# Kernel tuning notes

Hardware: AMD Instinct MI355X
Metric: run time of the kernel (lower is better)

## Reference

```python
import math
import jax, jax.numpy as jnp
import numpy as np

TOP_K, NC, ALPHA, BETA, EPS = 10, 80, 0.5, 6.0, 1e-9
IMG, STRIDES = 640, (8, 16, 32)


def _ciou(box1, box2, eps=1e-7):
    # box1: gt [bs,n,1,4], box2: pred [bs,1,na,4] -> [bs,n,na,1]
    b1x1, b1y1, b1x2, b1y2 = jnp.split(box1, 4, axis=-1)
    b2x1, b2y1, b2x2, b2y2 = jnp.split(box2, 4, axis=-1)
    w1, h1 = b1x2 - b1x1, b1y2 - b1y1 + eps
    w2, h2 = b2x2 - b2x1, b2y2 - b2y1 + eps
    inter = jnp.clip(jnp.minimum(b1x2, b2x2) - jnp.maximum(b1x1, b2x1), 0.0) * \
            jnp.clip(jnp.minimum(b1y2, b2y2) - jnp.maximum(b1y1, b2y1), 0.0)
    union = w1 * h1 + w2 * h2 - inter + eps
    iou = inter / union
    cw = jnp.maximum(b1x2, b2x2) - jnp.minimum(b1x1, b2x1)
    ch = jnp.maximum(b1y2, b2y2) - jnp.minimum(b1y1, b2y1)
    c2 = cw ** 2 + ch ** 2 + eps
    rho2 = ((b2x1 + b2x2 - b1x1 - b1x2) ** 2 + (b2y1 + b2y2 - b1y1 - b1y2) ** 2) / 4.0
    v = (4.0 / math.pi ** 2) * (jnp.arctan(w2 / h2) - jnp.arctan(w1 / h1)) ** 2
    alpha = jax.lax.stop_gradient(v / (v - iou + (1.0 + eps)))
    return iou - (rho2 / c2 + v * alpha)


def _assign(score, p_box, anchors, gt_labels, gt_box, mask):
    bs, na, nc = score.shape
    n = gt_box.shape[1]
    labels = gt_labels[..., 0].astype(jnp.int32)      # [bs,n]
    valid = mask > 0                                  # [bs,n,1] valid-gt mask
    # --- candidate mask: anchor center strictly inside gt box ---
    lt, rb = gt_box[..., :2], gt_box[..., 2:]
    d = jnp.concatenate([anchors[None, None] - lt[:, :, None],
                         rb[:, :, None] - anchors[None, None]], -1)  # [bs,n,na,4]
    mask_in_gts = d.min(-1) > 1e-9                    # [bs,n,na]
    mask_gts = mask_in_gts & valid
    # --- per-(gt,anchor) class score and CIoU overlap ---
    gathered = score[jnp.arange(bs)[:, None], :, labels]          # [bs,n,na]
    bbox_scores = jnp.where(mask_gts, gathered, 0.0)
    ov = _ciou(gt_box[:, :, None], p_box[:, None])[..., 0]        # [bs,n,na]
    overlaps = jnp.where(mask_gts, jnp.clip(ov, 0.0), 0.0)
    metric = jnp.where(mask_gts,
                       jnp.where(mask_gts, gathered, 1.0) ** ALPHA * overlaps ** BETA,
                       0.0)
    # --- top-k candidates per gt; suppress duplicated indices ---
    _, top_id = jax.lax.top_k(metric, TOP_K)          # [bs,n,TOP_K]
    top_id = jnp.where(valid, top_id, 0)
    bi = jnp.arange(bs)[:, None, None]
    ni = jnp.arange(n)[None, :, None]
    count = jnp.zeros((bs, n, na), jnp.int32).at[bi, ni, top_id].add(1)
    count = jnp.where(count > 1, 0, count)
    mask_pos = count.astype(metric.dtype) * mask_in_gts.astype(metric.dtype) * mask  # [bs,n,na]
    fg = mask_pos.sum(1)                              # [bs,na]
    # --- resolve anchors claimed by multiple gts via max overlap ---
    max_over = (jnp.arange(n)[None, :, None] == jnp.argmax(overlaps, 1)[:, None, :]).astype(metric.dtype)
    mask_pos = jnp.where(fg[:, None, :] > 1, max_over, mask_pos)
    fg = mask_pos.sum(1)
    # --- gather targets ---
    gt_idx = jnp.argmax(mask_pos, 1)                  # [bs,na]
    target_labels = jnp.clip(jnp.take_along_axis(labels, gt_idx, 1), 0)
    target_bboxes = jnp.take_along_axis(gt_box, gt_idx[..., None], 1)  # [bs,na,4]
    ts = jax.nn.one_hot(target_labels, NC, dtype=metric.dtype)
    ts = jnp.where(fg[..., None] > 0, ts, 0.0)
    # --- task-aligned score normalization ---
    metric = metric * mask_pos
    pos_metrics = metric.max(-1, keepdims=True)
    pos_overlaps = (overlaps * mask_pos).max(-1, keepdims=True)
    norm_metric = metric * pos_overlaps / (pos_metrics + EPS)
    target_scores = ts * norm_metric.max(1)[..., None]               # [bs,na,NC]
    return target_bboxes, target_scores, fg > 0


def setup_inputs() -> dict:
    key = jax.random.key(0)
    ks = jax.random.split(key, 8)
    bs, n_max = 16, 64
    # anchor points: grid cell centers for strides 8/16/32 at 640x640
    pts = []
    for s in STRIDES:
        g = IMG // s
        c = (jnp.arange(g, dtype=jnp.float32) + 0.5) * s
        gy, gx = jnp.meshgrid(c, c, indexing='ij')
        pts.append(jnp.stack([gx.ravel(), gy.ravel()], -1))
    anchors = jnp.concatenate(pts, 0)                 # [8400,2]
    na = anchors.shape[0]
    # predicted boxes centered near anchor points
    wh = jax.random.uniform(ks[0], (bs, na, 2), minval=8.0, maxval=128.0)
    ctr = anchors[None] + jax.random.normal(ks[1], (bs, na, 2)) * 4.0
    p_box = jnp.concatenate([ctr - wh / 2, ctr + wh / 2], -1)
    score = jax.random.uniform(ks[2], (bs, na, NC))
    # ground-truth boxes (valid x1<x2, y1<y2)
    gwh = jax.random.uniform(ks[3], (bs, n_max, 2), minval=16.0, maxval=256.0)
    gctr = jax.random.uniform(ks[4], (bs, n_max, 2), minval=0.0, maxval=float(IMG))
    gt_box = jnp.concatenate([gctr - gwh / 2, gctr + gwh / 2], -1)
    gt_labels = jax.random.randint(ks[5], (bs, n_max, 1), 0, NC)
    nvalid = jax.random.randint(ks[6], (bs, 1), 8, n_max + 1)
    mask = (jnp.arange(n_max)[None, :] < nvalid).astype(jnp.float32)[..., None]
    return {"score": score, "p_box": p_box, "anchors": anchors,
            "gt_labels": gt_labels, "gt_box": gt_box, "mask": mask}


def reference(score, p_box, anchors, gt_labels, gt_box, mask):
    return _assign(score, p_box, anchors, gt_labels, gt_box, mask)
```

## Files before the change

### kernel.cpp

```cpp
#include <hip/hip_runtime.h>
#include <math.h>

#define BS   16
#define NMAX 64
#define NA   8400
#define NCLS 80
#define TOPK 10
#define ROWS (BS * NMAX)
#define NSEG 16
#define SEGSZ 525
#define KPT  9
#define NCAND (NSEG * TOPK)

typedef unsigned long long u64;

__device__ __forceinline__ float ciou_clip(
    float gx1, float gy1, float gx2, float gy2, float at1, float area1,
    float px1, float py1, float px2, float py2, float at2, float area2)
{
    float iw = fminf(gx2, px2) - fmaxf(gx1, px1);
    float ih = fminf(gy2, py2) - fmaxf(gy1, py1);
    float inter = fmaxf(iw, 0.f) * fmaxf(ih, 0.f);
    float uni = area1 + area2 - inter + 1e-7f;
    float iou = inter / uni;
    float cw = fmaxf(gx2, px2) - fminf(gx1, px1);
    float ch = fmaxf(gy2, py2) - fminf(gy1, py1);
    float c2 = cw * cw + ch * ch + 1e-7f;
    float dx = px1 + px2 - gx1 - gx2;
    float dy = py1 + py2 - gy1 - gy2;
    float rho2 = (dx * dx + dy * dy) * 0.25f;
    float dat = at2 - at1;
    float v = (4.0f / (float)(M_PI * M_PI)) * dat * dat;
    float alpha = v / (v - iou + (1.0f + 1e-7f));
    return fmaxf(iou - (rho2 / c2 + v * alpha), 0.f);
}

__global__ __launch_bounds__(256) void k0_prep(
    const float* __restrict__ p_box,
    const float* __restrict__ gt_box,
    float2* __restrict__ at2tab,
    float*  __restrict__ at1r,
    float*  __restrict__ area1r,
    u64*    __restrict__ mask64,
    float*  __restrict__ pos_mt,
    float*  __restrict__ pos_ov)
{
    int i = blockIdx.x * 256 + threadIdx.x;
    if (i >= BS * NA) return;
    float4 pv = ((const float4*)p_box)[i];
    float w2 = pv.z - pv.x;
    float h2 = pv.w - pv.y + 1e-7f;
    at2tab[i] = make_float2(atanf(w2 / h2), w2 * h2);
    mask64[i] = 0ull;
    if (i < ROWS) {
        float4 gb = ((const float4*)gt_box)[i];
        float w1 = gb.z - gb.x;
        float h1 = gb.w - gb.y + 1e-7f;
        at1r[i] = atanf(w1 / h1);
        area1r[i] = w1 * h1;
        pos_mt[i] = 0.f;
        pos_ov[i] = 0.f;
    }
}

__global__ __launch_bounds__(256) void k1a(
    const float* __restrict__ score,
    const float* __restrict__ p_box,
    const float* __restrict__ anchors,
    const int*   __restrict__ gt_labels,
    const float* __restrict__ gt_box,
    const float* __restrict__ mask,
    const float2* __restrict__ at2tab,
    const float* __restrict__ at1r,
    const float* __restrict__ area1r,
    u64* __restrict__ cand_key)
{
    int row = blockIdx.x >> 2;
    if (mask[row] <= 0.f) return;
    int q   = blockIdx.x & 3;
    int b   = row >> 6;
    int lane = threadIdx.x & 63;
    int wid  = threadIdx.x >> 6;
    int seg  = q * 4 + wid;
    int base = seg * SEGSZ;

    float4 gb = ((const float4*)gt_box)[row];
    float at1 = at1r[row], area1 = area1r[row];
    int lbl = gt_labels[row];
    const float* sc = score + (size_t)b * NA * NCLS + lbl;
    const float4* pb = (const float4*)p_box + (size_t)b * NA;
    const float2* t2 = at2tab + (size_t)b * NA;
    const float2* an = (const float2*)anchors;

    u64 key[KPT];
#pragma unroll
    for (int k = 0; k < KPT; k++) {
        int ai = k * 64 + lane;
        u64 kk = 0ull;
        if (ai < SEGSZ) {
            int a = base + ai;
            float2 axy = an[a];
            float dmin = fminf(fminf(axy.x - gb.x, axy.y - gb.y),
                               fminf(gb.z - axy.x, gb.w - axy.y));
            float mt = 0.f;
            if (dmin > 1e-9f) {
                float4 pv = pb[a];
                float2 ta = t2[a];
                float ov = ciou_clip(gb.x, gb.y, gb.z, gb.w, at1, area1,
                                     pv.x, pv.y, pv.z, pv.w, ta.x, ta.y);
                float o2 = ov * ov;
                mt = sqrtf(sc[(size_t)a * NCLS]) * o2 * o2 * o2;
            }
            kk = ((u64)__float_as_uint(mt) << 32) | (unsigned)(~a);
        }
        key[k] = kk;
    }

    u64* ck = cand_key + (size_t)row * NCAND + seg * TOPK;
    for (int it = 0; it < TOPK; it++) {
        u64 m = key[0];
#pragma unroll
        for (int k = 1; k < KPT; k++) m = (key[k] > m) ? key[k] : m;
#pragma unroll
        for (int off = 1; off < 64; off <<= 1) {
            u64 o = __shfl_xor(m, off);
            if (o > m) m = o;
        }
        if (lane == it) ck[it] = m;
#pragma unroll
        for (int k = 0; k < KPT; k++) if (key[k] == m) key[k] = 0ull;
    }
}

__global__ __launch_bounds__(256) void k1b(
    const float* __restrict__ anchors,
    const float* __restrict__ p_box,
    const float* __restrict__ gt_box,
    const float* __restrict__ mask,
    const float2* __restrict__ at2tab,
    const float* __restrict__ at1r,
    const float* __restrict__ area1r,
    const u64*   __restrict__ cand_key,
    u64*   __restrict__ mask64,
    float* __restrict__ amt,
    float* __restrict__ aov)
{
    int row = blockIdx.x * 4 + (threadIdx.x >> 6);
    if (row >= ROWS) return;
    if (mask[row] <= 0.f) return;
    int lane = threadIdx.x & 63;
    int b = row >> 6, n = row & 63;
    const u64* ck = cand_key + (size_t)row * NCAND;
    u64 k0 = ck[lane];
    u64 k1 = ck[64 + lane];
    u64 k2 = (lane < 32) ? ck[128 + lane] : 0ull;

    float4 gb = ((const float4*)gt_box)[row];
    float at1 = at1r[row], area1 = area1r[row];

    for (int it = 0; it < TOPK; it++) {
        u64 m = (k0 > k1) ? k0 : k1;
        if (k2 > m) m = k2;
#pragma unroll
        for (int off = 1; off < 64; off <<= 1) {
            u64 o = __shfl_xor(m, off);
            if (o > m) m = o;
        }
        if (lane == it) {
            int a = (int)(~(unsigned)(m & 0xffffffffu));
            float mt = __uint_as_float((unsigned)(m >> 32));
            float2 axy = ((const float2*)anchors)[a];
            float dmin = fminf(fminf(axy.x - gb.x, axy.y - gb.y),
                               fminf(gb.z - axy.x, gb.w - axy.y));
            if (dmin > 1e-9f) {
                size_t i = (size_t)b * NA + a;
                atomicOr(&mask64[i], 1ull << n);
                float4 pv = ((const float4*)p_box)[i];
                float2 ta = at2tab[i];
                float ov = ciou_clip(gb.x, gb.y, gb.z, gb.w, at1, area1,
                                     pv.x, pv.y, pv.z, pv.w, ta.x, ta.y);
                amt[i] = mt;
                aov[i] = ov;
            }
        }
        if (k0 == m) k0 = 0ull;
        if (k1 == m) k1 = 0ull;
        if (k2 == m) k2 = 0ull;
    }
}

__global__ __launch_bounds__(256) void k3_resolve(
    const float* __restrict__ score,
    const float* __restrict__ p_box,
    const float* __restrict__ anchors,
    const int*   __restrict__ gt_labels,
    const float* __restrict__ gt_box,
    const float* __restrict__ mask,
    const float2* __restrict__ at2tab,
    const float* __restrict__ at1r,
    const float* __restrict__ area1r,
    const u64*   __restrict__ mask64,
    const float* __restrict__ amt,
    const float* __restrict__ aov,
    int* __restrict__ gt_idx,
    unsigned char* __restrict__ fg_arr,
    float* __restrict__ tgt_mt,
    float* __restrict__ out_bbox,
    float* __restrict__ out_fg,
    float* __restrict__ pos_mt,
    float* __restrict__ pos_ov)
{
    int i = blockIdx.x * 256 + threadIdx.x;
    if (i >= BS * NA) return;
    int b = i / NA, a = i - b * NA;
    u64 bits = mask64[i];
    int fg0 = __popcll(bits);
    int gi = 0, fg = (fg0 > 0);
    float mt = 0.f, ov = 0.f;
    if (fg0 == 1) {
        gi = __ffsll(bits) - 1;
        mt = amt[i];
        ov = aov[i];
    } else if (fg0 > 1) {
        float2 axy = ((const float2*)anchors)[a];
        float4 pv = ((const float4*)p_box)[i];
        float2 ta = at2tab[i];
        const float* mrow = mask + b * NMAX;
        float best = -1.f; int argn = 0;
        for (int nn = 0; nn < NMAX; nn++) {
            float v = 0.f;
            if (mrow[nn] > 0.f) {
                int r = b * NMAX + nn;
                float4 gb = ((const float4*)gt_box)[r];
                float dmin = fminf(fminf(axy.x - gb.x, axy.y - gb.y),
                                   fminf(gb.z - axy.x, gb.w - axy.y));
                if (dmin > 1e-9f)
                    v = ciou_clip(gb.x, gb.y, gb.z, gb.w, at1r[r], area1r[r],
                                  pv.x, pv.y, pv.z, pv.w, ta.x, ta.y);
            }
            if (v > best) { best = v; argn = nn; }
        }
        gi = argn;
        ov = fmaxf(best, 0.f);
        int lbl = gt_labels[b * NMAX + argn]; if (lbl < 0) lbl = 0;
        float gath = score[((size_t)b * NA + a) * NCLS + lbl];
        float o2 = ov * ov;
        mt = sqrtf(gath) * o2 * o2 * o2;
    }
    int r = b * NMAX + gi;
    gt_idx[i] = gi;
    fg_arr[i] = (unsigned char)fg;
    tgt_mt[i] = mt;
    out_fg[i] = fg ? 1.f : 0.f;
    ((float4*)out_bbox)[i] = ((const float4*)gt_box)[r];
    if (fg) {
        atomicMax((int*)&pos_mt[r], __float_as_int(mt));
        atomicMax((int*)&pos_ov[r], __float_as_int(ov));
    }
}

__global__ __launch_bounds__(256) void k5_full(
    const int*   __restrict__ gt_idx,
    const unsigned char* __restrict__ fg_arr,
    const float* __restrict__ tgt_mt,
    const int*   __restrict__ gt_labels,
    const float* __restrict__ pos_mt,
    const float* __restrict__ pos_ov,
    float4* __restrict__ out_scores)
{
    int i = blockIdx.x * 256 + threadIdx.x;
    if (i >= BS * NA * (NCLS / 4)) return;
    int ba = i / (NCLS / 4);
    int c4 = (i - ba * (NCLS / 4)) * 4;
    float4 o = make_float4(0.f, 0.f, 0.f, 0.f);
    if (fg_arr[ba]) {
        int b = ba / NA;
        int r = b * NMAX + gt_idx[ba];
        int lbl = gt_labels[r]; if (lbl < 0) lbl = 0;
        if (lbl >= c4 && lbl < c4 + 4) {
            float val = tgt_mt[ba] * pos_ov[r] / (pos_mt[r] + 1e-9f);
            if (lbl == c4)     o.x = val;
            if (lbl == c4 + 1) o.y = val;
            if (lbl == c4 + 2) o.z = val;
            if (lbl == c4 + 3) o.w = val;
        }
    }
    out_scores[i] = o;
}

extern "C" void kernel_launch(void* const* d_in, const int* in_sizes, int n_in,
                              void* d_out, int out_size, void* d_ws, size_t ws_size,
                              hipStream_t stream) {
    (void)in_sizes; (void)n_in; (void)out_size; (void)ws_size;
    const float* score     = (const float*)d_in[0];
    const float* p_box     = (const float*)d_in[1];
    const float* anchors   = (const float*)d_in[2];
    const int*   gt_labels = (const int*)d_in[3];
    const float* gt_box    = (const float*)d_in[4];
    const float* mask      = (const float*)d_in[5];

    char* w = (char*)d_ws;
    float2* at2tab  = (float2*)w;              w += (size_t)BS * NA * 8;
    u64*   mask64   = (u64*)w;                 w += (size_t)BS * NA * 8;
    u64*   cand_key = (u64*)w;                 w += (size_t)ROWS * NCAND * 8;
    float* amt      = (float*)w;               w += (size_t)BS * NA * 4;
    float* aov      = (float*)w;               w += (size_t)BS * NA * 4;
    int*   gt_idx   = (int*)w;                 w += (size_t)BS * NA * 4;
    float* tgt_mt   = (float*)w;               w += (size_t)BS * NA * 4;
    float* at1r     = (float*)w;               w += (size_t)ROWS * 4;
    float* area1r   = (float*)w;               w += (size_t)ROWS * 4;
    float* pos_mt   = (float*)w;               w += (size_t)ROWS * 4;
    float* pos_ov   = (float*)w;               w += (size_t)ROWS * 4;
    unsigned char* fg_arr = (unsigned char*)w; w += (size_t)BS * NA;

    float* out_bbox   = (float*)d_out;
    float* out_scores = out_bbox + (size_t)BS * NA * 4;
    float* out_fg     = out_scores + (size_t)BS * NA * NCLS;

    hipLaunchKernelGGL(k0_prep, dim3((BS * NA + 255) / 256), dim3(256), 0, stream,
                       p_box, gt_box, at2tab, at1r, area1r, mask64, pos_mt, pos_ov);
    hipLaunchKernelGGL(k1a, dim3(ROWS * 4), dim3(256), 0, stream,
                       score, p_box, anchors, gt_labels, gt_box, mask,
                       at2tab, at1r, area1r, cand_key);
    hipLaunchKernelGGL(k1b, dim3(ROWS / 4), dim3(256), 0, stream,
                       anchors, p_box, gt_box, mask, at2tab, at1r, area1r,
                       cand_key, mask64, amt, aov);
    hipLaunchKernelGGL(k3_resolve, dim3((BS * NA + 255) / 256), dim3(256), 0, stream,
                       score, p_box, anchors, gt_labels, gt_box, mask,
                       at2tab, at1r, area1r, mask64, amt, aov,
                       gt_idx, fg_arr, tgt_mt, out_bbox, out_fg, pos_mt, pos_ov);
    hipLaunchKernelGGL(k5_full, dim3((BS * NA * (NCLS / 4) + 255) / 256), dim3(256), 0, stream,
                       gt_idx, fg_arr, tgt_mt, gt_labels, pos_mt, pos_ov,
                       (float4*)out_scores);
}
```

Before: 169.3 us.

## Restrict top-k candidate scan to anchor grid cells inside each GT box

Replaces the two-pass segmented top-k (full 8400-anchor scan per GT plus a merge kernel) with a single kernel that computes each GT box's anchor-grid bounding ranges on the three stride levels and evaluates only anchors inside them. Each lane keeps a sorted 10-entry list, and a wavefront merge picks the final top-k. Zero-metric filler keys from the first anchor row are inserted to mimic the reference tie-breaking on zero metrics. This removes most of the wasted per-anchor work, the candidate buffer traffic and one launch. The cost is relying on the anchor grid layout being analytic and a reduced parallelism of one wave per GT row.

```diff
diff --git a/kernel.cpp b/kernel.cpp
--- a/kernel.cpp
+++ b/kernel.cpp
@@ -7,10 +7,6 @@
 #define NCLS 80
 #define TOPK 10
 #define ROWS (BS * NMAX)
-#define NSEG 16
-#define SEGSZ 525
-#define KPT  9
-#define NCAND (NSEG * TOPK)
 
 typedef unsigned long long u64;
 
@@ -63,26 +59,31 @@
     }
 }
 
-__global__ __launch_bounds__(256) void k1a(
+#define INS10(kk)                                                         \
+    if ((kk) > L[9]) {                                                    \
+        L[9] = (kk);                                                      \
+        _Pragma("unroll")                                                 \
+        for (int q = 9; q >= 1; q--)                                      \
+            if (L[q] > L[q-1]) { u64 tt = L[q-1]; L[q-1] = L[q]; L[q] = tt; } \
+    }
+
+__global__ __launch_bounds__(256) void k1_rows(
     const float* __restrict__ score,
     const float* __restrict__ p_box,
-    const float* __restrict__ anchors,
     const int*   __restrict__ gt_labels,
     const float* __restrict__ gt_box,
     const float* __restrict__ mask,
     const float2* __restrict__ at2tab,
     const float* __restrict__ at1r,
     const float* __restrict__ area1r,
-    u64* __restrict__ cand_key)
-{
-    int row = blockIdx.x >> 2;
+    u64*   __restrict__ mask64,
+    float* __restrict__ amt,
+    float* __restrict__ aov)
+{
+    int row  = blockIdx.x * 4 + (threadIdx.x >> 6);
+    int lane = threadIdx.x & 63;
     if (mask[row] <= 0.f) return;
-    int q   = blockIdx.x & 3;
-    int b   = row >> 6;
-    int lane = threadIdx.x & 63;
-    int wid  = threadIdx.x >> 6;
-    int seg  = q * 4 + wid;
-    int base = seg * SEGSZ;
+    int b = row >> 6, n = row & 63;
 
     float4 gb = ((const float4*)gt_box)[row];
     float at1 = at1r[row], area1 = area1r[row];
@@ -90,102 +91,104 @@
     const float* sc = score + (size_t)b * NA * NCLS + lbl;
     const float4* pb = (const float4*)p_box + (size_t)b * NA;
     const float2* t2 = at2tab + (size_t)b * NA;
-    const float2* an = (const float2*)anchors;
-
-    u64 key[KPT];
+
+    int ilo0 = max(0,  (int)floorf(gb.x * 0.125f   - 0.5f));
+    int ihi0 = min(79, (int)ceilf (gb.z * 0.125f   - 0.5f));
+    int jlo0 = max(0,  (int)floorf(gb.y * 0.125f   - 0.5f));
+    int jhi0 = min(79, (int)ceilf (gb.w * 0.125f   - 0.5f));
+    int ilo1 = max(0,  (int)floorf(gb.x * 0.0625f  - 0.5f));
+    int ihi1 = min(39, (int)ceilf (gb.z * 0.0625f  - 0.5f));
+    int jlo1 = max(0,  (int)floorf(gb.y * 0.0625f  - 0.5f));
+    int jhi1 = min(39, (int)ceilf (gb.w * 0.0625f  - 0.5f));
+    int ilo2 = max(0,  (int)floorf(gb.x * 0.03125f - 0.5f));
+    int ihi2 = min(19, (int)ceilf (gb.z * 0.03125f - 0.5f));
+    int jlo2 = max(0,  (int)floorf(gb.y * 0.03125f - 0.5f));
+    int jhi2 = min(19, (int)ceilf (gb.w * 0.03125f - 0.5f));
+    int nx0 = max(0, ihi0 - ilo0 + 1), ny0 = max(0, jhi0 - jlo0 + 1);
+    int nx1 = max(0, ihi1 - ilo1 + 1), ny1 = max(0, jhi1 - jlo1 + 1);
+    int nx2 = max(0, ihi2 - ilo2 + 1), ny2 = max(0, jhi2 - jlo2 + 1);
+    int c0 = nx0 * ny0;
+    int c1 = c0 + nx1 * ny1;
+    int T  = c1 + nx2 * ny2;
+
+    u64 L[10];
 #pragma unroll
-    for (int k = 0; k < KPT; k++) {
-        int ai = k * 64 + lane;
-        u64 kk = 0ull;
-        if (ai < SEGSZ) {
-            int a = base + ai;
-            float2 axy = an[a];
-            float dmin = fminf(fminf(axy.x - gb.x, axy.y - gb.y),
-                               fminf(gb.z - axy.x, gb.w - axy.y));
-            float mt = 0.f;
-            if (dmin > 1e-9f) {
-                float4 pv = pb[a];
-                float2 ta = t2[a];
-                float ov = ciou_clip(gb.x, gb.y, gb.z, gb.w, at1, area1,
-                                     pv.x, pv.y, pv.z, pv.w, ta.x, ta.y);
-                float o2 = ov * ov;
-                mt = sqrtf(sc[(size_t)a * NCLS]) * o2 * o2 * o2;
-            }
-            kk = ((u64)__float_as_uint(mt) << 32) | (unsigned)(~a);
-        }
-        key[k] = kk;
-    }
-
-    u64* ck = cand_key + (size_t)row * NCAND + seg * TOPK;
+    for (int q = 0; q < 10; q++) L[q] = 0ull;
+
+    for (int t = lane; t < T; t += 64) {
+        bool ge1 = t >= c0, ge2 = t >= c1;
+        int local = t - (ge2 ? c1 : (ge1 ? c0 : 0));
+        int nxl  = ge2 ? nx2  : (ge1 ? nx1  : nx0);
+        int ilol = ge2 ? ilo2 : (ge1 ? ilo1 : ilo0);
+        int jlol = ge2 ? jlo2 : (ge1 ? jlo1 : jlo0);
+        int g    = ge2 ? 20   : (ge1 ? 40   : 80);
+        int off  = ge2 ? 8000 : (ge1 ? 6400 : 0);
+        float s  = ge2 ? 32.f : (ge1 ? 16.f : 8.f);
+        int jj = local / nxl;
+        int ii = local - jj * nxl;
+        int i = ilol + ii, j = jlol + jj;
+        int a = off + j * g + i;
+        float ax = ((float)i + 0.5f) * s, ay = ((float)j + 0.5f) * s;
+        float dmin = fminf(fminf(ax - gb.x, ay - gb.y),
+                           fminf(gb.z - ax, gb.w - ay));
+        if (dmin > 1e-9f) {
+            float4 pv = pb[a];
+            float2 ta = t2[a];
+            float ov = ciou_clip(gb.x, gb.y, gb.z, gb.w, at1, area1,
+                                 pv.x, pv.y, pv.z, pv.w, ta.x, ta.y);
+            float o2 = ov * ov;
+            float mt = sqrtf(sc[(size_t)a * NCLS]) * o2 * o2 * o2;
+            u64 kk = ((u64)__float_as_uint(mt) << 32) | (unsigned)(~a);
+            INS10(kk)
+        }
+    }
+    {
+        float ax = (float)lane * 8.f + 4.f, ay = 4.f;
+        float dmin = fminf(fminf(ax - gb.x, ay - gb.y),
+                           fminf(gb.z - ax, gb.w - ay));
+        if (!(dmin > 1e-9f)) {
+            u64 kk = (u64)(unsigned)(~lane);
+            INS10(kk)
+        }
+    }
+
+    u64 winkey = 0ull;
     for (int it = 0; it < TOPK; it++) {
-        u64 m = key[0];
+        u64 m = L[0];
 #pragma unroll
-        for (int k = 1; k < KPT; k++) m = (key[k] > m) ? key[k] : m;
+        for (int o = 1; o < 64; o <<= 1) {
+            u64 v = __shfl_xor(m, o);
+            if (v > m) m = v;
+        }
+        if (lane == it) winkey = m;
+        if (L[0] == m) {
 #pragma unroll
-        for (int off = 1; off < 64; off <<= 1) {
-            u64 o = __shfl_xor(m, off);
-            if (o > m) m = o;
-        }
-        if (lane == it) ck[it] = m;
-#pragma unroll
-        for (int k = 0; k < KPT; k++) if (key[k] == m) key[k] = 0ull;
-    }
-}
-
-__global__ __launch_bounds__(256) void k1b(
-    const float* __restrict__ anchors,
-    const float* __restrict__ p_box,
-    const float* __restrict__ gt_box,
-    const float* __restrict__ mask,
-    const float2* __restrict__ at2tab,
-    const float* __restrict__ at1r,
-    const float* __restrict__ area1r,
-    const u64*   __restrict__ cand_key,
-    u64*   __restrict__ mask64,
-    float* __restrict__ amt,
-    float* __restrict__ aov)
-{
-    int row = blockIdx.x * 4 + (threadIdx.x >> 6);
-    if (row >= ROWS) return;
-    if (mask[row] <= 0.f) return;
-    int lane = threadIdx.x & 63;
-    int b = row >> 6, n = row & 63;
-    const u64* ck = cand_key + (size_t)row * NCAND;
-    u64 k0 = ck[lane];
-    u64 k1 = ck[64 + lane];
-    u64 k2 = (lane < 32) ? ck[128 + lane] : 0ull;
-
-    float4 gb = ((const float4*)gt_box)[row];
-    float at1 = at1r[row], area1 = area1r[row];
-
-    for (int it = 0; it < TOPK; it++) {
-        u64 m = (k0 > k1) ? k0 : k1;
-        if (k2 > m) m = k2;
-#pragma unroll
-        for (int off = 1; off < 64; off <<= 1) {
-            u64 o = __shfl_xor(m, off);
-            if (o > m) m = o;
-        }
-        if (lane == it) {
-            int a = (int)(~(unsigned)(m & 0xffffffffu));
-            float mt = __uint_as_float((unsigned)(m >> 32));
-            float2 axy = ((const float2*)anchors)[a];
-            float dmin = fminf(fminf(axy.x - gb.x, axy.y - gb.y),
-                               fminf(gb.z - axy.x, gb.w - axy.y));
-            if (dmin > 1e-9f) {
-                size_t i = (size_t)b * NA + a;
-                atomicOr(&mask64[i], 1ull << n);
-                float4 pv = ((const float4*)p_box)[i];
-                float2 ta = at2tab[i];
-                float ov = ciou_clip(gb.x, gb.y, gb.z, gb.w, at1, area1,
-                                     pv.x, pv.y, pv.z, pv.w, ta.x, ta.y);
-                amt[i] = mt;
-                aov[i] = ov;
-            }
-        }
-        if (k0 == m) k0 = 0ull;
-        if (k1 == m) k1 = 0ull;
-        if (k2 == m) k2 = 0ull;
+            for (int q = 0; q < 9; q++) L[q] = L[q + 1];
+            L[9] = 0ull;
+        }
+    }
+
+    if (lane < TOPK && winkey) {
+        int a = (int)(~(unsigned)(winkey & 0xffffffffu));
+        float mt = __uint_as_float((unsigned)(winkey >> 32));
+        bool l2 = a >= 8000, l1 = (a >= 6400) && !l2;
+        int loc = a - (l2 ? 8000 : (l1 ? 6400 : 0));
+        int g   = l2 ? 20 : (l1 ? 40 : 80);
+        float s = l2 ? 32.f : (l1 ? 16.f : 8.f);
+        int j = loc / g, i = loc - j * g;
+        float ax = ((float)i + 0.5f) * s, ay = ((float)j + 0.5f) * s;
+        float dmin = fminf(fminf(ax - gb.x, ay - gb.y),
+                           fminf(gb.z - ax, gb.w - ay));
+        if (dmin > 1e-9f) {
+            size_t idx = (size_t)b * NA + a;
+            atomicOr(&mask64[idx], 1ull << n);
+            float4 pv = pb[a];
+            float2 ta = t2[a];
+            float ov = ciou_clip(gb.x, gb.y, gb.z, gb.w, at1, area1,
+                                 pv.x, pv.y, pv.z, pv.w, ta.x, ta.y);
+            amt[idx] = mt;
+            aov[idx] = ov;
+        }
     }
 }
 
@@ -231,11 +234,11 @@
             float v = 0.f;
             if (mrow[nn] > 0.f) {
                 int r = b * NMAX + nn;
-                float4 gb = ((const float4*)gt_box)[r];
-                float dmin = fminf(fminf(axy.x - gb.x, axy.y - gb.y),
-                                   fminf(gb.z - axy.x, gb.w - axy.y));
+                float4 gbv = ((const float4*)gt_box)[r];
+                float dmin = fminf(fminf(axy.x - gbv.x, axy.y - gbv.y),
+                                   fminf(gbv.z - axy.x, gbv.w - axy.y));
                 if (dmin > 1e-9f)
-                    v = ciou_clip(gb.x, gb.y, gb.z, gb.w, at1r[r], area1r[r],
+                    v = ciou_clip(gbv.x, gbv.y, gbv.z, gbv.w, at1r[r], area1r[r],
                                   pv.x, pv.y, pv.z, pv.w, ta.x, ta.y);
             }
             if (v > best) { best = v; argn = nn; }
@@ -302,7 +305,6 @@
     char* w = (char*)d_ws;
     float2* at2tab  = (float2*)w;              w += (size_t)BS * NA * 8;
     u64*   mask64   = (u64*)w;                 w += (size_t)BS * NA * 8;
-    u64*   cand_key = (u64*)w;                 w += (size_t)ROWS * NCAND * 8;
     float* amt      = (float*)w;               w += (size_t)BS * NA * 4;
     float* aov      = (float*)w;               w += (size_t)BS * NA * 4;
     int*   gt_idx   = (int*)w;                 w += (size_t)BS * NA * 4;
@@ -319,12 +321,9 @@
 
     hipLaunchKernelGGL(k0_prep, dim3((BS * NA + 255) / 256), dim3(256), 0, stream,
                        p_box, gt_box, at2tab, at1r, area1r, mask64, pos_mt, pos_ov);
-    hipLaunchKernelGGL(k1a, dim3(ROWS * 4), dim3(256), 0, stream,
-                       score, p_box, anchors, gt_labels, gt_box, mask,
-                       at2tab, at1r, area1r, cand_key);
-    hipLaunchKernelGGL(k1b, dim3(ROWS / 4), dim3(256), 0, stream,
-                       anchors, p_box, gt_box, mask, at2tab, at1r, area1r,
-                       cand_key, mask64, amt, aov);
+    hipLaunchKernelGGL(k1_rows, dim3(ROWS / 4), dim3(256), 0, stream,
+                       score, p_box, gt_labels, gt_box, mask,
+                       at2tab, at1r, area1r, mask64, amt, aov);
     hipLaunchKernelGGL(k3_resolve, dim3((BS * NA + 255) / 256), dim3(256), 0, stream,
                        score, p_box, anchors, gt_labels, gt_box, mask,
                        at2tab, at1r, area1r, mask64, amt, aov,
```

New measurement: 150.7 us. 11.0% less time.
